# Optimization experiments

Hardware: AMD Instinct MI355X
Metric: run time of the kernel (lower is better)

Reference implementation:

```python
import jax, jax.numpy as jnp
import numpy as np

N_E = 1024
N_H = 16
SZ = N_E // N_H  # 64
NEG_INF = float('-inf')


def _layernorm(x, g, b):
    # Faithful to source: unbiased variance (ddof=1), eps added AFTER sqrt.
    mu = jnp.mean(x, axis=-1, keepdims=True)
    v = jnp.var(x, axis=-1, keepdims=True, ddof=1)
    xn = (x - mu) / (jnp.sqrt(v) + 1e-8)
    return g * xn + b


def setup_inputs() -> dict:
    key = jax.random.key(0)
    ks = jax.random.split(key, 16)
    s = 0.02
    x = jax.random.normal(ks[0], (4, 2048, N_E), dtype=jnp.float32)
    # Stacked per-head Q/K/V linears: weight [H, sz, n_e], bias [H, sz]
    Wq = jax.random.normal(ks[1], (N_H, SZ, N_E), dtype=jnp.float32) * s
    bq = jax.random.normal(ks[2], (N_H, SZ), dtype=jnp.float32) * s
    Wk = jax.random.normal(ks[3], (N_H, SZ, N_E), dtype=jnp.float32) * s
    bk = jax.random.normal(ks[4], (N_H, SZ), dtype=jnp.float32) * s
    Wv = jax.random.normal(ks[5], (N_H, SZ, N_E), dtype=jnp.float32) * s
    bv = jax.random.normal(ks[6], (N_H, SZ), dtype=jnp.float32) * s
    Wo = jax.random.normal(ks[7], (N_E, N_E), dtype=jnp.float32) * s
    bo = jax.random.normal(ks[8], (N_E,), dtype=jnp.float32) * s
    g1 = jnp.ones((N_E,), dtype=jnp.float32)
    be1 = jnp.zeros((N_E,), dtype=jnp.float32)
    g2 = jnp.ones((N_E,), dtype=jnp.float32)
    be2 = jnp.zeros((N_E,), dtype=jnp.float32)
    W1 = jax.random.normal(ks[9], (4 * N_E, N_E), dtype=jnp.float32) * s
    bf1 = jax.random.normal(ks[10], (4 * N_E,), dtype=jnp.float32) * s
    W2 = jax.random.normal(ks[11], (N_E, 4 * N_E), dtype=jnp.float32) * s
    bf2 = jax.random.normal(ks[12], (N_E,), dtype=jnp.float32) * s
    return dict(x=x, Wq=Wq, bq=bq, Wk=Wk, bk=bk, Wv=Wv, bv=bv, Wo=Wo, bo=bo,
                g1=g1, be1=be1, g2=g2, be2=be2, W1=W1, bf1=bf1, W2=W2, bf2=bf2)


def reference(x, Wq, bq, Wk, bk, Wv, bv, Wo, bo, g1, be1, g2, be2, W1, bf1, W2, bf2):
    # --- MHA sublayer ---
    xn = _layernorm(x, g1, be1)
    # Q/K/V for all heads at once: [B, H, S, sz]
    Q = jnp.einsum('bsd,hkd->bhsk', xn, Wq) + bq[None, :, None, :]
    K = jnp.einsum('bsd,hkd->bhsk', xn, Wk) + bk[None, :, None, :]
    V = jnp.einsum('bsd,hkd->bhsk', xn, Wv) + bv[None, :, None, :]
    scores = jnp.einsum('bhqk,bhmk->bhqm', Q, K) / (SZ ** 0.5)  # [B,H,S,S]
    # Faithful to source quirk: mask where tril(scores) == 0
    masked = jnp.where(jnp.tril(scores) == 0, NEG_INF, scores)
    attn = jax.nn.softmax(masked, axis=-1)
    o = jnp.einsum('bhqm,bhmk->bhqk', attn, V)  # [B,H,S,sz]
    B, H, S, _ = o.shape
    o = jnp.transpose(o, (0, 2, 1, 3)).reshape(B, S, H * SZ)  # concat heads
    x = x + o @ Wo.T + bo
    # --- FFN sublayer (dropout = identity in eval) ---
    xn2 = _layernorm(x, g2, be2)
    h = jax.nn.gelu(xn2 @ W1.T + bf1, approximate=False)
    x = x + h @ W2.T + bf2
    return x
```

## Files before the change

### kernel.cpp

```cpp
#include <hip/hip_runtime.h>
#include <math.h>


typedef unsigned short u16;
typedef unsigned int u32;
typedef __attribute__((ext_vector_type(8))) short bf16x8;
typedef __attribute__((ext_vector_type(4))) float f32x4;

#define T_TOK 8192
#define DM    1024
#define SEQ   2048
#define PST   88

__device__ __forceinline__ u16 f2bf(float f) {
  union { float f; unsigned int u; } c; c.f = f;
  unsigned int u = c.u + 0x7fffu + ((c.u >> 16) & 1u);
  return (u16)(u >> 16);
}

__device__ __forceinline__ u32 pk2(float a, float b) {
  return (u32)f2bf(a) | ((u32)f2bf(b) << 16);
}

__device__ __forceinline__ float bf2f(short s) {
  union { float f; unsigned int u; } c; c.u = ((u32)(u16)s) << 16;
  return c.f;
}

__device__ __forceinline__ void gload16(const void* gp, void* lp) {
  __builtin_amdgcn_global_load_lds(
      (const __attribute__((address_space(1))) void*)gp,
      (__attribute__((address_space(3))) void*)lp, 16, 0, 0);
}

__device__ __forceinline__ float gelu_tanh(float v) {
  float u = 0.7978845608f * (v + 0.044715f * v * v * v);
  return v / (1.0f + __expf(-2.0f * u));
}

__global__ __launch_bounds__(256) void prep_kernel(
    const float* __restrict__ x, const float* __restrict__ g,
    const float* __restrict__ b, u16* __restrict__ xnB,
    const float* __restrict__ Wq, const float* __restrict__ Wk,
    const float* __restrict__ Wv, const float* __restrict__ Wo,
    const float* __restrict__ W1, const float* __restrict__ W2,
    u16* __restrict__ WqkvB, u16* __restrict__ WoB,
    u16* __restrict__ W1B, u16* __restrict__ W2B,
    const float* __restrict__ bq, const float* __restrict__ bk,
    const float* __restrict__ bv, float* __restrict__ bqkv) {
  __shared__ float red[4];
  const int bid = blockIdx.x, tid = threadIdx.x;
  if (bid < 8192) {
    const int l = tid & 63, w = tid >> 6;
    const size_t row = bid;
    float4 v = reinterpret_cast<const float4*>(x + row * DM)[tid];
    float s = v.x + v.y + v.z + v.w;
#pragma unroll
    for (int off = 1; off < 64; off <<= 1) s += __shfl_xor(s, off, 64);
    if (l == 0) red[w] = s;
    __syncthreads();
    float mu = (red[0] + red[1] + red[2] + red[3]) * (1.0f / 1024.0f);
    float dx = v.x - mu, dy = v.y - mu, dz = v.z - mu, dw = v.w - mu;
    float ss = dx * dx + dy * dy + dz * dz + dw * dw;
#pragma unroll
    for (int off = 1; off < 64; off <<= 1) ss += __shfl_xor(ss, off, 64);
    __syncthreads();
    if (l == 0) red[w] = ss;
    __syncthreads();
    float var = (red[0] + red[1] + red[2] + red[3]) * (1.0f / 1023.0f);
    float inv = 1.0f / (sqrtf(var) + 1e-8f);
    const int c = tid * 4;
    u16* o = xnB + row * DM + c;
    o[0] = f2bf(dx * inv * g[c + 0] + b[c + 0]);
    o[1] = f2bf(dy * inv * g[c + 1] + b[c + 1]);
    o[2] = f2bf(dz * inv * g[c + 2] + b[c + 2]);
    o[3] = f2bf(dw * inv * g[c + 3] + b[c + 3]);
  } else if (bid < 10240) {
    for (int i = (bid - 8192) * 256 + tid; i < 3145728; i += 2048 * 256) {
      const float* s; u16* d; int j;
      if (i < 262144)       { s = Wq; d = WqkvB;           j = i; }
      else if (i < 524288)  { s = Wk; d = WqkvB + 1048576; j = i - 262144; }
      else if (i < 786432)  { s = Wv; d = WqkvB + 2097152; j = i - 524288; }
      else if (i < 1048576) { s = Wo; d = WoB;             j = i - 786432; }
      else if (i < 2097152) { s = W1; d = W1B;             j = i - 1048576; }
      else                  { s = W2; d = W2B;             j = i - 2097152; }
      float4 v = reinterpret_cast<const float4*>(s)[j];
      ushort4 o = { f2bf(v.x), f2bf(v.y), f2bf(v.z), f2bf(v.w) };
      reinterpret_cast<ushort4*>(d)[j] = o;
    }
  } else {
    int i = (bid - 10240) * 256 + tid;
    float val = (i < 1024) ? bq[i] : (i < 2048) ? bk[i - 1024] : bv[i - 2048];
    bqkv[i] = val;
  }
}

__global__ __launch_bounds__(256) void ln_kernel(const float* __restrict__ x,
    const float* __restrict__ g, const float* __restrict__ b, u16* __restrict__ out) {
  __shared__ float red[4];
  const int tid = threadIdx.x, l = tid & 63, w = tid >> 6;
  const size_t row = blockIdx.x;
  float4 v = reinterpret_cast<const float4*>(x + row * DM)[tid];
  float s = v.x + v.y + v.z + v.w;
#pragma unroll
  for (int off = 1; off < 64; off <<= 1) s += __shfl_xor(s, off, 64);
  if (l == 0) red[w] = s;
  __syncthreads();
  float mu = (red[0] + red[1] + red[2] + red[3]) * (1.0f / 1024.0f);
  float dx = v.x - mu, dy = v.y - mu, dz = v.z - mu, dw = v.w - mu;
  float ss = dx * dx + dy * dy + dz * dz + dw * dw;
#pragma unroll
  for (int off = 1; off < 64; off <<= 1) ss += __shfl_xor(ss, off, 64);
  __syncthreads();
  if (l == 0) red[w] = ss;
  __syncthreads();
  float var = (red[0] + red[1] + red[2] + red[3]) * (1.0f / 1023.0f);
  float inv = 1.0f / (sqrtf(var) + 1e-8f);
  const int c = tid * 4;
  u16* o = out + row * DM + c;
  o[0] = f2bf(dx * inv * g[c + 0] + b[c + 0]);
  o[1] = f2bf(dy * inv * g[c + 1] + b[c + 1]);
  o[2] = f2bf(dz * inv * g[c + 2] + b[c + 2]);
  o[3] = f2bf(dw * inv * g[c + 3] + b[c + 3]);
}

__global__ __launch_bounds__(256) void vt_kernel(const u16* __restrict__ vr,
                                                 u16* __restrict__ vt) {
  __shared__ u16 t[64][72];
  const int st = blockIdx.x;
  const int bh = blockIdx.y, b = bh >> 4, h = bh & 15;
  const int tid = threadIdx.x;
  const int ss = tid >> 3, dc = (tid & 7) * 8;
  const u16* src = vr + (size_t)(b * SEQ + st * 64) * 1024 + h * 64;
  *(bf16x8*)&t[ss][dc]      = *(const bf16x8*)(src + (size_t)ss * 1024 + dc);
  *(bf16x8*)&t[ss + 32][dc] = *(const bf16x8*)(src + (size_t)(ss + 32) * 1024 + dc);
  __syncthreads();
  const int d0 = tid >> 3, s0 = (tid & 7) * 8;
  u16* dst = vt + (size_t)bh * 64 * SEQ + st * 64;
  bf16x8 o0, o1;
#pragma unroll
  for (int i = 0; i < 8; ++i) {
    o0[i] = (short)t[s0 + i][d0];
    o1[i] = (short)t[s0 + i][d0 + 32];
  }
  *(bf16x8*)(dst + (size_t)d0 * SEQ + s0)        = o0;
  *(bf16x8*)(dst + (size_t)(d0 + 32) * SEQ + s0) = o1;
}

template <int EPI, int BM>
__global__ __launch_bounds__(512) void gemm8p(const u16* __restrict__ A,
    const u16* __restrict__ Bw, const float* __restrict__ bias,
    const float* res, void* Cout, void* aux, int M, int N, int K, int gx) {
  constexpr int MI  = BM / 32;
  constexpr int AMI = MI / 2;
  constexpr int VC  = (BM == 256) ? 6 : 5;
  __shared__ __align__(16) u16 ldsA[2][2][BM * 32];
  __shared__ __align__(16) u16 ldsB[2][2][256 * 32];
  const int tid = threadIdx.x;
  const int l = tid & 63;
  const int w = tid >> 6;
  const int wm = w >> 2, wn = w & 3;
  const int lr = l & 15, lg = l >> 4;

  const int nb = gridDim.x;
  const int q = nb >> 3, r = nb & 7;
  const int xcd = blockIdx.x & 7, jj = blockIdx.x >> 3;
  const int lid = (xcd < r ? xcd * (q + 1) : r * (q + 1) + (xcd - r) * q) + jj;
  const int stid = lid >> 5, pos = lid & 31;
  const int nstx = gx >> 2;
  const int stx = stid % nstx, sty = stid / nstx;
  const int bx = stx * 4 + (pos & 3), by = sty * 8 + (pos >> 2);
  const int m0 = by * BM, n0 = bx * 256;

  const int Dl = tid * 16;
  const int Ls = Dl ^ (((Dl >> 7) & 3) << 4);
  const int srow = Ls >> 6;
  const int scol = (Ls & 63) >> 1;
  const u16* aS0 = A  + (size_t)(m0 + srow) * K + scol;
  const u16* aS1 = aS0 + (size_t)128 * K;
  const u16* bS0 = Bw + (size_t)(n0 + srow) * K + scol;
  const u16* bS1 = bS0 + (size_t)128 * K;

  const int sx = ((lr >> 1) & 3) << 4;
  const int aBase = (wm * (BM / 2) + lr) * 64 + ((lg * 16) ^ sx);
  const int bBase = (wn * 64 + lr) * 64 + ((lg * 16) ^ sx);

  f32x4 acc[MI][4];
#pragma unroll
  for (int i = 0; i < MI; ++i)
#pragma unroll
    for (int j = 0; j < 4; ++j) acc[i][j] = f32x4{0.f, 0.f, 0.f, 0.f};
  bf16x8 bv[2][4];

  const int NT = K >> 6;
  const int NI = NT >> 1;

  auto stA = [&](int d, int ks, int tile) {
    u16* dst = &ldsA[d][ks][tid * 8];
    const int ko = tile * 64 + ks * 32;
    gload16(aS0 + ko, dst);
    if constexpr (BM == 256) gload16(aS1 + ko, dst + 4096);
  };
  auto stB = [&](int d, int ks, int tile) {
    u16* dst = &ldsB[d][ks][tid * 8];
    const int ko = tile * 64 + ks * 32;
    gload16(bS0 + ko, dst);
    gload16(bS1 + ko, dst + 4096);
  };

  stB(0, 0, 0); stB(0, 1, 0); stA(0, 0, 0); stA(0, 1, 0);
  stB(1, 0, 1); stB(1, 1, 1); stA(1, 0, 1);
  asm volatile("s_waitcnt vmcnt(%0)" :: "i"(VC) : "memory");
  __builtin_amdgcn_sched_barrier(0);
  __builtin_amdgcn_s_barrier();

#define PHASE(DBUF, KS, MH, READB, STAGE, ENDV)                               \
  {                                                                           \
    const char* abuf = (const char*)&ldsA[DBUF][KS][0];                       \
    const char* bbuf = (const char*)&ldsB[DBUF][KS][0];                       \
    bf16x8 av[AMI];                                                           \
    _Pragma("unroll")                                                         \
    for (int i = 0; i < AMI; ++i)                                             \
      av[i] = *(const bf16x8*)(abuf + aBase + ((MH) * AMI + i) * 1024);       \
    if (READB) {                                                              \
      _Pragma("unroll")                                                       \
      for (int ni = 0; ni < 4; ++ni)                                          \
        bv[KS][ni] = *(const bf16x8*)(bbuf + bBase + ni * 1024);              \
    }                                                                         \
    STAGE;                                                                    \
    __builtin_amdgcn_s_barrier();                                             \
    asm volatile("s_waitcnt lgkmcnt(0)" ::: "memory");                        \
    __builtin_amdgcn_sched_barrier(0);                                        \
    __builtin_amdgcn_s_setprio(1);                                            \
    _Pragma("unroll")                                                         \
    for (int i = 0; i < AMI; ++i)                                             \
      _Pragma("unroll")                                                       \
      for (int ni = 0; ni < 4; ++ni)                                          \
        acc[(MH) * AMI + i][ni] = __builtin_amdgcn_mfma_f32_16x16x32_bf16(    \
            av[i], bv[KS][ni], acc[(MH) * AMI + i][ni], 0, 0, 0);             \
    __builtin_amdgcn_s_setprio(0);                                            \
    ENDV;                                                                     \
    __builtin_amdgcn_s_barrier();                                             \
  }

#define ENDV_CNT                                                              \
  {                                                                           \
    if (t + 1 < NI) {                                                         \
      asm volatile("s_waitcnt vmcnt(%0)" :: "i"(VC) : "memory");              \
    } else {                                                                  \
      asm volatile("s_waitcnt vmcnt(0)" ::: "memory");                        \
    }                                                                         \
    __builtin_amdgcn_sched_barrier(0);                                        \
  }

  for (int t = 0; t < NI; ++t) {
    const int t2 = 2 * t;
    const bool s0 = (t2 + 2 < NT);
    const bool s1 = (t2 + 3 < NT);
    PHASE(0, 0, 0, 1, { stA(1, 1, t2 + 1); }, {});
    PHASE(0, 1, 0, 1, { if (s0) stB(0, 0, t2 + 2); }, {});
    PHASE(0, 0, 1, 0, { if (s0) stB(0, 1, t2 + 2); }, {});
    PHASE(0, 1, 1, 0, { if (s0) stA(0, 0, t2 + 2); }, ENDV_CNT);
    PHASE(1, 0, 0, 1, { if (s0) stA(0, 1, t2 + 2); }, {});
    PHASE(1, 1, 0, 1, { if (s1) stB(1, 0, t2 + 3); }, {});
    PHASE(1, 0, 1, 0, { if (s1) stB(1, 1, t2 + 3); }, {});
    PHASE(1, 1, 1, 0, { if (s1) stA(1, 0, t2 + 3); }, ENDV_CNT);
  }
#undef PHASE
#undef ENDV_CNT

  float bs[4];
#pragma unroll
  for (int ni = 0; ni < 4; ++ni) bs[ni] = bias[n0 + wn * 64 + ni * 16 + lr];
#pragma unroll
  for (int mi = 0; mi < MI; ++mi) {
#pragma unroll
    for (int j = 0; j < 4; ++j) {
      const int rr = m0 + wm * (BM / 2) + mi * 16 + lg * 4 + j;
#pragma unroll
      for (int ni = 0; ni < 4; ++ni) {
        const int c = n0 + wn * 64 + ni * 16 + lr;
        float v = acc[mi][ni][j] + bs[ni];
        if constexpr (EPI == 0) {
          if (n0 >= 2048) {
            ((u16*)aux)[(size_t)rr * 1024 + (c - 2048)] = f2bf(v);
          } else {
            ((u16*)Cout)[(size_t)rr * 2048 + c] = f2bf(v);
          }
        } else if constexpr (EPI == 1) {
          const size_t idx = (size_t)rr * N + c;
          ((float*)Cout)[idx] = v + res[idx];
        } else {
          const size_t idx = (size_t)rr * N + c;
          ((u16*)Cout)[idx] = f2bf(gelu_tanh(v));
        }
      }
    }
  }
}

__global__ __launch_bounds__(512) void attn_kernel(const u16* __restrict__ qk,
    const u16* __restrict__ vt, u16* __restrict__ obuf) {
  __shared__ __align__(16) u16 ldsK[3][64 * 64];
  __shared__ __align__(16) u16 ldsV[3][64 * 64];
  __shared__ __align__(16) u16 ldsP[8][2][16 * PST];
  const int tid = threadIdx.x, l = tid & 63, w = tid >> 6;
  const int lr = l & 15, lg = l >> 4;
  const int lid = (blockIdx.x & 7) * 32 + (blockIdx.x >> 3);
  const int bh = lid >> 2, bx = lid & 3;
  const int b = bh >> 4, h = bh & 15;
  const u16* qbase = qk + (size_t)b * SEQ * 2048 + h * 64;
  const u16* kbase = qk + (size_t)b * SEQ * 2048 + 1024 + h * 64;
  const u16* vbase = vt + (size_t)bh * 64 * SEQ;

  const int srow = tid >> 3;
  const int scb  = ((tid & 7) * 16) ^ ((srow & 7) << 4);
  const int sel  = scb >> 1;

  auto stageKV = [&](int t) {
    const int bi = t % 3;
    gload16(kbase + (size_t)(t * 64 + srow) * 2048 + sel, &ldsK[bi][tid * 8]);
    gload16(vbase + (size_t)srow * SEQ + t * 64 + sel,    &ldsV[bi][tid * 8]);
  };

#pragma unroll
  for (int half = 0; half < 2; ++half) {
    const int qt = half ? (7 - bx) : bx;
    const int q0 = qt * 256 + w * 32;
    bf16x8 qf[2][2];
#pragma unroll
    for (int mi = 0; mi < 2; ++mi)
#pragma unroll
      for (int ks = 0; ks < 2; ++ks) {
        bf16x8 raw = *(const bf16x8*)(qbase +
            (size_t)(q0 + mi * 16 + lr) * 2048 + ks * 32 + lg * 8);
        bf16x8 sc8;
#pragma unroll
        for (int i = 0; i < 8; ++i) sc8[i] = (short)f2bf(bf2f(raw[i]) * 0.125f);
        qf[mi][ks] = sc8;
      }

    f32x4 o[2][4];
#pragma unroll
    for (int mi = 0; mi < 2; ++mi)
#pragma unroll
      for (int nd = 0; nd < 4; ++nd) o[mi][nd] = f32x4{0.f, 0.f, 0.f, 0.f};
    float m_[2] = {-1e30f, -1e30f}, ls[2] = {0.f, 0.f};

    const int nt = 4 * qt + 4;
    const int qmaxw = q0 + 31;

    stageKV(0);

    for (int kt = 0; kt < nt; ++kt) {
      if (kt + 1 < nt) {
        stageKV(kt + 1);
        asm volatile("s_waitcnt vmcnt(2)" ::: "memory");
      } else {
        asm volatile("s_waitcnt vmcnt(0)" ::: "memory");
      }
      __builtin_amdgcn_s_barrier();
      __builtin_amdgcn_sched_barrier(0);
      const u16* bK = &ldsK[kt % 3][0];
      const u16* bV = &ldsV[kt % 3][0];

      if (kt * 64 <= qmaxw) {
        f32x4 sc[2][4];
#pragma unroll
        for (int mi = 0; mi < 2; ++mi)
#pragma unroll
          for (int ni = 0; ni < 4; ++ni) sc[mi][ni] = f32x4{0.f, 0.f, 0.f, 0.f};
#pragma unroll
        for (int ks = 0; ks < 2; ++ks)
#pragma unroll
          for (int ni = 0; ni < 4; ++ni) {
            const int r2 = ni * 16 + lr;
            const int cb = (r2 << 7) + ((ks * 64 + lg * 16) ^ ((r2 & 7) << 4));
            bf16x8 kf = *(const bf16x8*)&bK[cb >> 1];
            sc[0][ni] = __builtin_amdgcn_mfma_f32_16x16x32_bf16(kf, qf[0][ks], sc[0][ni], 0, 0, 0);
            sc[1][ni] = __builtin_amdgcn_mfma_f32_16x16x32_bf16(kf, qf[1][ks], sc[1][ni], 0, 0, 0);
          }

        if (kt * 64 + 63 > q0) {
#pragma unroll
          for (int mi = 0; mi < 2; ++mi) {
            const int qa = q0 + mi * 16 + lr;
#pragma unroll
            for (int ni = 0; ni < 4; ++ni)
#pragma unroll
              for (int j = 0; j < 4; ++j) {
                const int ka = kt * 64 + ni * 16 + lg * 4 + j;
                if (ka > qa) sc[mi][ni][j] = -1e30f;
              }
          }
        }

#pragma unroll
        for (int mi = 0; mi < 2; ++mi) {
          float mx = sc[mi][0][0];
#pragma unroll
          for (int ni = 0; ni < 4; ++ni)
#pragma unroll
            for (int j = 0; j < 4; ++j) mx = fmaxf(mx, sc[mi][ni][j]);
          mx = fmaxf(mx, __shfl_xor(mx, 16, 64));
          mx = fmaxf(mx, __shfl_xor(mx, 32, 64));
          if (!__all(mx <= m_[mi] + 8.0f)) {
            const float newm = fmaxf(m_[mi], mx);
            const float alpha = __expf(m_[mi] - newm);
            m_[mi] = newm;
            ls[mi] *= alpha;
#pragma unroll
            for (int nd = 0; nd < 4; ++nd) {
              o[mi][nd][0] *= alpha; o[mi][nd][1] *= alpha;
              o[mi][nd][2] *= alpha; o[mi][nd][3] *= alpha;
            }
          }
          float ps = 0.f;
#pragma unroll
          for (int ni = 0; ni < 4; ++ni) {
            float p0 = __expf(sc[mi][ni][0] - m_[mi]);
            float p1 = __expf(sc[mi][ni][1] - m_[mi]);
            float p2 = __expf(sc[mi][ni][2] - m_[mi]);
            float p3 = __expf(sc[mi][ni][3] - m_[mi]);
            ps += (p0 + p1) + (p2 + p3);
            u32 w0 = pk2(p0, p1), w1 = pk2(p2, p3);
            *(uint2*)&ldsP[w][mi][lr * PST + ni * 16 + lg * 4] = make_uint2(w0, w1);
          }
          ps += __shfl_xor(ps, 16, 64);
          ps += __shfl_xor(ps, 32, 64);
          ls[mi] += ps;
        }

#pragma unroll
        for (int ks = 0; ks < 2; ++ks) {
          bf16x8 pf0 = *(const bf16x8*)&ldsP[w][0][lr * PST + ks * 32 + lg * 8];
          bf16x8 pf1 = *(const bf16x8*)&ldsP[w][1][lr * PST + ks * 32 + lg * 8];
#pragma unroll
          for (int nd = 0; nd < 4; ++nd) {
            const int r2 = nd * 16 + lr;
            const int cb = (r2 << 7) + ((ks * 64 + lg * 16) ^ ((r2 & 7) << 4));
            bf16x8 vf = *(const bf16x8*)&bV[cb >> 1];
            o[0][nd] = __builtin_amdgcn_mfma_f32_16x16x32_bf16(vf, pf0, o[0][nd], 0, 0, 0);
            o[1][nd] = __builtin_amdgcn_mfma_f32_16x16x32_bf16(vf, pf1, o[1][nd], 0, 0, 0);
          }
        }
      }
    }
    __builtin_amdgcn_s_barrier();

#pragma unroll
    for (int mi = 0; mi < 2; ++mi) {
      const float inv = 1.0f / ls[mi];
      const int qrow = q0 + mi * 16 + lr;
      u16* op = obuf + (size_t)(b * SEQ + qrow) * DM + h * 64 + lg * 4;
#pragma unroll
      for (int nd = 0; nd < 4; ++nd) {
        ushort4 pk = { f2bf(o[mi][nd][0] * inv), f2bf(o[mi][nd][1] * inv),
                       f2bf(o[mi][nd][2] * inv), f2bf(o[mi][nd][3] * inv) };
        *(ushort4*)(op + nd * 16) = pk;
      }
    }
  }
}

extern "C" void kernel_launch(void* const* d_in, const int* in_sizes, int n_in,
                              void* d_out, int out_size, void* d_ws, size_t ws_size,
                              hipStream_t stream) {
  const float* x   = (const float*)d_in[0];
  const float* Wq  = (const float*)d_in[1];
  const float* bq  = (const float*)d_in[2];
  const float* Wk  = (const float*)d_in[3];
  const float* bk  = (const float*)d_in[4];
  const float* Wv  = (const float*)d_in[5];
  const float* bv  = (const float*)d_in[6];
  const float* Wo  = (const float*)d_in[7];
  const float* bo  = (const float*)d_in[8];
  const float* g1  = (const float*)d_in[9];
  const float* be1 = (const float*)d_in[10];
  const float* g2  = (const float*)d_in[11];
  const float* be2 = (const float*)d_in[12];
  const float* W1  = (const float*)d_in[13];
  const float* bf1 = (const float*)d_in[14];
  const float* W2  = (const float*)d_in[15];
  const float* bf2 = (const float*)d_in[16];
  float* out = (float*)d_out;

  char* ws = (char*)d_ws;
  size_t off = 0;
  auto alloc = [&](size_t bytes) {
    char* p = ws + off;
    off += (bytes + 255) & ~(size_t)255;
    return p;
  };
  u16* xnB = (u16*)alloc((size_t)T_TOK * DM * 2);
  u16* D    = (u16*)alloc((size_t)T_TOK * 4096 * 2);
  u16* qkB  = D;
  u16* VTg  = D + (size_t)T_TOK * 2048;
  u16* Vrow = D + (size_t)T_TOK * 3072;
  u16* oB   = Vrow;
  u16* HB   = D;
  u16*   WqkvB = (u16*)alloc((size_t)3072 * 1024 * 2);
  u16*   WoB   = (u16*)alloc((size_t)1024 * 1024 * 2);
  u16*   W1B   = (u16*)alloc((size_t)4096 * 1024 * 2);
  u16*   W2B   = (u16*)alloc((size_t)1024 * 4096 * 2);
  float* bqkv  = (float*)alloc(3072 * 4);

  prep_kernel<<<10252, 256, 0, stream>>>(x, g1, be1, xnB,
                                         Wq, Wk, Wv, Wo, W1, W2,
                                         WqkvB, WoB, W1B, W2B,
                                         bq, bk, bv, bqkv);

  gemm8p<0, 128><<<768, 512, 0, stream>>>(xnB, WqkvB, bqkv, nullptr,
                                          qkB, Vrow, T_TOK, 3072, 1024, 12);
  vt_kernel<<<dim3(32, 64), 256, 0, stream>>>(Vrow, VTg);
  attn_kernel<<<256, 512, 0, stream>>>(qkB, VTg, oB);
  gemm8p<1, 128><<<256, 512, 0, stream>>>(oB, WoB, bo, x,
                                          out, nullptr, T_TOK, 1024, 1024, 4);

  ln_kernel<<<T_TOK, 256, 0, stream>>>(out, g2, be2, xnB);
  gemm8p<2, 256><<<512, 512, 0, stream>>>(xnB, W1B, bf1, nullptr,
                                          HB, nullptr, T_TOK, 4096, 1024, 16);
  gemm8p<1, 128><<<256, 512, 0, stream>>>(HB, W2B, bf2, out,
                                          out, nullptr, T_TOK, 1024, 4096, 4);
}
```

Before: 383.0 us.

## Fuse V transpose into QKV GEMM epilogue via shared-memory staging

Removes the separate vt_kernel. The QKV GEMM's V-column blocks now write their tile transposed through shared memory directly into the head-major V^T layout. The separate LDS arrays become one shared buffer so the epilogue can reuse it as transpose scratch. This drops a full write and re-read of the V tensor and one kernel launch, at the cost of an extra barrier and an LDS round trip in the GEMM epilogue for those blocks.

```diff
diff --git a/kernel.cpp b/kernel.cpp
--- a/kernel.cpp
+++ b/kernel.cpp
@@ -11,6 +11,7 @@
 #define DM    1024
 #define SEQ   2048
 #define PST   88
+#define TST   136
 
 __device__ __forceinline__ u16 f2bf(float f) {
   union { float f; unsigned int u; } c; c.f = f;
@@ -124,29 +125,6 @@
   o[3] = f2bf(dw * inv * g[c + 3] + b[c + 3]);
 }
 
-__global__ __launch_bounds__(256) void vt_kernel(const u16* __restrict__ vr,
-                                                 u16* __restrict__ vt) {
-  __shared__ u16 t[64][72];
-  const int st = blockIdx.x;
-  const int bh = blockIdx.y, b = bh >> 4, h = bh & 15;
-  const int tid = threadIdx.x;
-  const int ss = tid >> 3, dc = (tid & 7) * 8;
-  const u16* src = vr + (size_t)(b * SEQ + st * 64) * 1024 + h * 64;
-  *(bf16x8*)&t[ss][dc]      = *(const bf16x8*)(src + (size_t)ss * 1024 + dc);
-  *(bf16x8*)&t[ss + 32][dc] = *(const bf16x8*)(src + (size_t)(ss + 32) * 1024 + dc);
-  __syncthreads();
-  const int d0 = tid >> 3, s0 = (tid & 7) * 8;
-  u16* dst = vt + (size_t)bh * 64 * SEQ + st * 64;
-  bf16x8 o0, o1;
-#pragma unroll
-  for (int i = 0; i < 8; ++i) {
-    o0[i] = (short)t[s0 + i][d0];
-    o1[i] = (short)t[s0 + i][d0 + 32];
-  }
-  *(bf16x8*)(dst + (size_t)d0 * SEQ + s0)        = o0;
-  *(bf16x8*)(dst + (size_t)(d0 + 32) * SEQ + s0) = o1;
-}
-
 template <int EPI, int BM>
 __global__ __launch_bounds__(512) void gemm8p(const u16* __restrict__ A,
     const u16* __restrict__ Bw, const float* __restrict__ bias,
@@ -154,8 +132,7 @@
   constexpr int MI  = BM / 32;
   constexpr int AMI = MI / 2;
   constexpr int VC  = (BM == 256) ? 6 : 5;
-  __shared__ __align__(16) u16 ldsA[2][2][BM * 32];
-  __shared__ __align__(16) u16 ldsB[2][2][256 * 32];
+  __shared__ __align__(16) u16 shm[BM * 128 + 256 * 128];
   const int tid = threadIdx.x;
   const int l = tid & 63;
   const int w = tid >> 6;
@@ -196,13 +173,13 @@
   const int NI = NT >> 1;
 
   auto stA = [&](int d, int ks, int tile) {
-    u16* dst = &ldsA[d][ks][tid * 8];
+    u16* dst = shm + (d * 2 + ks) * (BM * 32) + tid * 8;
     const int ko = tile * 64 + ks * 32;
     gload16(aS0 + ko, dst);
     if constexpr (BM == 256) gload16(aS1 + ko, dst + 4096);
   };
   auto stB = [&](int d, int ks, int tile) {
-    u16* dst = &ldsB[d][ks][tid * 8];
+    u16* dst = shm + BM * 128 + (d * 2 + ks) * (256 * 32) + tid * 8;
     const int ko = tile * 64 + ks * 32;
     gload16(bS0 + ko, dst);
     gload16(bS1 + ko, dst + 4096);
@@ -216,8 +193,9 @@
 
 #define PHASE(DBUF, KS, MH, READB, STAGE, ENDV)                               \
   {                                                                           \
-    const char* abuf = (const char*)&ldsA[DBUF][KS][0];                       \
-    const char* bbuf = (const char*)&ldsB[DBUF][KS][0];                       \
+    const char* abuf = (const char*)(shm + ((DBUF) * 2 + (KS)) * (BM * 32));  \
+    const char* bbuf =                                                        \
+        (const char*)(shm + BM * 128 + ((DBUF) * 2 + (KS)) * (256 * 32));     \
     bf16x8 av[AMI];                                                           \
     _Pragma("unroll")                                                         \
     for (int i = 0; i < AMI; ++i)                                             \
@@ -272,6 +250,36 @@
   float bs[4];
 #pragma unroll
   for (int ni = 0; ni < 4; ++ni) bs[ni] = bias[n0 + wn * 64 + ni * 16 + lr];
+
+  if constexpr (EPI == 0) {
+    if (n0 >= 2048) {
+      u16* ldsT = shm;
+#pragma unroll
+      for (int mi = 0; mi < MI; ++mi)
+#pragma unroll
+        for (int ni = 0; ni < 4; ++ni) {
+          const int c = wn * 64 + ni * 16 + lr;
+          const int r0 = wm * (BM / 2) + mi * 16 + lg * 4;
+          ushort4 pk = { f2bf(acc[mi][ni][0] + bs[ni]),
+                         f2bf(acc[mi][ni][1] + bs[ni]),
+                         f2bf(acc[mi][ni][2] + bs[ni]),
+                         f2bf(acc[mi][ni][3] + bs[ni]) };
+          *(ushort4*)&ldsT[c * TST + r0] = pk;
+        }
+      __syncthreads();
+      const int b0 = m0 >> 11, s0b = m0 & 2047;
+      const int cc = tid >> 1, hf = tid & 1;
+      const int hd = (n0 - 2048) + cc, hh = hd >> 6, dd = hd & 63;
+      u16* dst = (u16*)aux +
+                 (((size_t)(b0 * 16 + hh) * 64 + dd) << 11) + s0b + hf * 64;
+      const u16* srcT = &ldsT[cc * TST + hf * 64];
+#pragma unroll
+      for (int i2 = 0; i2 < 8; ++i2)
+        *(bf16x8*)(dst + i2 * 8) = *(const bf16x8*)(srcT + i2 * 8);
+      return;
+    }
+  }
+
 #pragma unroll
   for (int mi = 0; mi < MI; ++mi) {
 #pragma unroll
@@ -282,11 +290,7 @@
         const int c = n0 + wn * 64 + ni * 16 + lr;
         float v = acc[mi][ni][j] + bs[ni];
         if constexpr (EPI == 0) {
-          if (n0 >= 2048) {
-            ((u16*)aux)[(size_t)rr * 1024 + (c - 2048)] = f2bf(v);
-          } else {
-            ((u16*)Cout)[(size_t)rr * 2048 + c] = f2bf(v);
-          }
+          ((u16*)Cout)[(size_t)rr * 2048 + c] = f2bf(v);
         } else if constexpr (EPI == 1) {
           const size_t idx = (size_t)rr * N + c;
           ((float*)Cout)[idx] = v + res[idx];
@@ -496,8 +500,7 @@
   u16* D    = (u16*)alloc((size_t)T_TOK * 4096 * 2);
   u16* qkB  = D;
   u16* VTg  = D + (size_t)T_TOK * 2048;
-  u16* Vrow = D + (size_t)T_TOK * 3072;
-  u16* oB   = Vrow;
+  u16* oB   = D + (size_t)T_TOK * 3072;
   u16* HB   = D;
   u16*   WqkvB = (u16*)alloc((size_t)3072 * 1024 * 2);
   u16*   WoB   = (u16*)alloc((size_t)1024 * 1024 * 2);
@@ -511,8 +514,7 @@
                                          bq, bk, bv, bqkv);
 
   gemm8p<0, 128><<<768, 512, 0, stream>>>(xnB, WqkvB, bqkv, nullptr,
-                                          qkB, Vrow, T_TOK, 3072, 1024, 12);
-  vt_kernel<<<dim3(32, 64), 256, 0, stream>>>(Vrow, VTg);
+                                          qkB, VTg, T_TOK, 3072, 1024, 12);
   attn_kernel<<<256, 512, 0, stream>>>(qkB, VTg, oB);
   gemm8p<1, 128><<<256, 512, 0, stream>>>(oB, WoB, bo, x,
                                           out, nullptr, T_TOK, 1024, 1024, 4);
```

Result: faster. 362.8 us (-5.3%).
